# Kernel tuning notes

Hardware: AMD Instinct MI355X
Metric: run time of the kernel (lower is better)

## Reference

```python
import jax, jax.numpy as jnp
import numpy as np

B, S, D, H = 4, 2048, 1024, 16
Dh = D // H
MAX_WAVELENGTH = 10000.0


def apply_rope(x, positions, head_dim):
    # x: [B, S, H, Dh], positions: [B, S]
    fraction = 2.0 * jnp.arange(head_dim // 2, dtype=jnp.float32) / head_dim
    timescale = MAX_WAVELENGTH ** fraction                     # [Dh/2]
    sinusoid = positions[..., None].astype(jnp.float32) / timescale  # [B, S, Dh/2]
    sinusoid = sinusoid[..., None, :]                          # [B, S, 1, Dh/2]
    sin, cos = jnp.sin(sinusoid), jnp.cos(sinusoid)
    first, second = jnp.split(x, 2, axis=-1)
    out = jnp.concatenate([first * cos - second * sin,
                           second * cos + first * sin], axis=-1)
    return out.astype(x.dtype)


def setup_inputs() -> dict:
    key = jax.random.key(0)
    k0, k1, k2, k3, k4 = jax.random.split(key, 5)
    inputs = jax.random.normal(k0, (B, S, D), dtype=jnp.float32)
    segment_positions = jnp.broadcast_to(jnp.arange(S, dtype=jnp.int32), (B, S))
    # causal mask, broadcastable over heads: [B, 1, S, S]
    mask = jnp.broadcast_to(jnp.tril(jnp.ones((S, S), dtype=bool))[None, None], (B, 1, S, S))
    std = 0.02
    w_q = jax.random.normal(k1, (D, H, Dh), dtype=jnp.float32) * std
    w_k = jax.random.normal(k2, (D, H, Dh), dtype=jnp.float32) * std
    w_v = jax.random.normal(k3, (D, H, Dh), dtype=jnp.float32) * std
    w_out = jax.random.normal(k4, (H, Dh, D), dtype=jnp.float32) * std
    return {"inputs": inputs, "w_q": w_q, "w_k": w_k, "w_v": w_v,
            "w_out": w_out, "segment_positions": segment_positions, "mask": mask}


def reference(inputs, w_q, w_k, w_v, w_out, segment_positions, mask):
    # QKV projections: [B, S, D] x [D, H, Dh] -> [B, S, H, Dh]
    q = jnp.einsum('bsd,dhk->bshk', inputs, w_q)
    k = jnp.einsum('bsd,dhk->bshk', inputs, w_k)
    v = jnp.einsum('bsd,dhk->bshk', inputs, w_v)
    q = apply_rope(q, segment_positions, Dh)
    k = apply_rope(k, segment_positions, Dh)
    q = q / jnp.sqrt(jnp.asarray(Dh, dtype=q.dtype))
    attn = jnp.einsum('bqhd,bkhd->bhqk', q, k)                 # [B, H, S, S]
    big_neg = jnp.finfo(attn.dtype).min
    attn = jnp.where(mask, attn, big_neg)
    attn = jax.nn.softmax(attn, axis=-1)
    x = jnp.einsum('bhqk,bkhd->bqhd', attn, v)                 # [B, S, H, Dh]
    return jnp.einsum('bqhd,hdm->bqm', x, w_out)               # [B, S, D]
```

## Files before the change

kernel.cpp:

```cpp
#include <hip/hip_runtime.h>
#include <stdint.h>
#include <math.h>

#define S_LEN 2048
#define DMODEL 1024
#define NHEAD 16
#define DHEAD 64
#define BATCH 4
#define MROWS (BATCH * S_LEN)

typedef __attribute__((ext_vector_type(8))) short bf16x8;
typedef __attribute__((ext_vector_type(4))) float f32x4;

#define MFMA16(a, b, c) __builtin_amdgcn_mfma_f32_16x16x32_bf16(a, b, c, 0, 0, 0)

__device__ __forceinline__ unsigned short f2b(float f) {
  union { float f; unsigned u; } v; v.f = f;
  unsigned u = v.u;
  return (unsigned short)((u + 0x7FFFu + ((u >> 16) & 1u)) >> 16);
}
__device__ __forceinline__ unsigned pkrn(float a, float b) {
  unsigned ua = __float_as_uint(a) + 0x8000u;
  unsigned ub = __float_as_uint(b) + 0x8000u;
  return __builtin_amdgcn_perm(ub, ua, 0x07060302);
}

__device__ __forceinline__ void async16(const void* g, void* l) {
  __builtin_amdgcn_global_load_lds((const __attribute__((address_space(1))) void*)g,
                                   (__attribute__((address_space(3))) void*)l,
                                   16, 0, 0);
}

struct PrepArgs {
  const float4* x; unsigned short* xb; int n4; int cvtBlocks;
  const float* s[4]; unsigned short* d[4];
};
__global__ __launch_bounds__(256) void prep_kernel(PrepArgs p) {
  __shared__ float T[64][65];
  const int bid = blockIdx.x;
  const int t = threadIdx.x;
  if (bid < p.cvtBlocks) {
    int i = bid * 256 + t;
    if (i < p.n4) {
      float4 v = p.x[i];
      ushort4 o;
      o.x = f2b(v.x); o.y = f2b(v.y); o.z = f2b(v.z); o.w = f2b(v.w);
      *(ushort4*)(p.xb + 4 * (size_t)i) = o;
    }
    return;
  }
  const int tb = bid - p.cvtBlocks;
  const int z = tb >> 8;
  const int rem = tb & 255;
  const int r0 = (rem >> 4) * 64, c0 = (rem & 15) * 64;
  const float* in = p.s[z];
  unsigned short* out = p.d[z];
  int c = t & 63, rr = t >> 6;
#pragma unroll
  for (int i = 0; i < 16; i++) {
    int r = i * 4 + rr;
    T[r][c] = in[(size_t)(r0 + r) * 1024 + c0 + c];
  }
  __syncthreads();
  int r2 = t & 63, cc = t >> 6;
#pragma unroll
  for (int i = 0; i < 16; i++) {
    int c2 = i * 4 + cc;
    out[(size_t)(c0 + c2) * 1024 + r0 + r2] = f2b(T[r2][c2]);
  }
}

__global__ __launch_bounds__(256) void gemm_qkv(const unsigned short* __restrict__ A,
                                                const unsigned short* __restrict__ Bt,
                                                unsigned short* __restrict__ Qr,
                                                unsigned short* __restrict__ Kr,
                                                unsigned short* __restrict__ Vt,
                                                const int* __restrict__ pos) {
  constexpr int K = 1024;
  __shared__ unsigned short As[128 * 64];
  __shared__ unsigned short Bs[128 * 64];
  const int bm = blockIdx.y * 128, bn = blockIdx.x * 128;
  const int t = threadIdx.x;
  const int wave = t >> 6, lane = t & 63, quad = lane >> 4, l16 = lane & 15;
  const int wm = (wave >> 1) * 64, wn = (wave & 1) * 64;
  f32x4 acc[4][4] = {};
  const int srow = lane >> 3;
  const int gcol = (((lane & 7) ^ srow)) * 8;
  const unsigned short* Ag = A + (size_t)(bm + wave * 32 + srow) * K + gcol;
  const unsigned short* Bg = Bt + (size_t)(bn + wave * 32 + srow) * K + gcol;
  unsigned short* AsW = &As[(wave * 32) * 64];
  unsigned short* BsW = &Bs[(wave * 32) * 64];
  const int rsw = l16 & 7;

  for (int k0 = 0; k0 < K; k0 += 64) {
    __syncthreads();
#pragma unroll
    for (int i = 0; i < 4; i++) {
      async16(Ag + (size_t)(i * 8) * K + k0, AsW + i * 8 * 64);
      async16(Bg + (size_t)(i * 8) * K + k0, BsW + i * 8 * 64);
    }
    __syncthreads();
#pragma unroll
    for (int kk = 0; kk < 2; kk++) {
      const int sl = ((kk * 4 + quad) ^ rsw) << 3;
      bf16x8 af[4], bfr[4];
#pragma unroll
      for (int mt = 0; mt < 4; mt++)
        af[mt] = *(const bf16x8*)&As[(wm + mt * 16 + l16) * 64 + sl];
#pragma unroll
      for (int nt = 0; nt < 4; nt++)
        bfr[nt] = *(const bf16x8*)&Bs[(wn + nt * 16 + l16) * 64 + sl];
#pragma unroll
      for (int mt = 0; mt < 4; mt++)
#pragma unroll
        for (int nt = 0; nt < 4; nt++)
          acc[mt][nt] = MFMA16(af[mt], bfr[nt], acc[mt][nt]);
    }
  }

  const int cb = bn + wn;
  if (cb >= 2048) {
    const int h = (cb - 2048) >> 6;
#pragma unroll
    for (int mt = 0; mt < 4; mt++)
#pragma unroll
      for (int nt = 0; nt < 4; nt++) {
        int row = bm + wm + mt * 16 + quad * 4;
        int b = row >> 11, s = row & (S_LEN - 1);
        int dh = nt * 16 + l16;
        ushort4 w4;
        w4.x = f2b(acc[mt][nt][0]); w4.y = f2b(acc[mt][nt][1]);
        w4.z = f2b(acc[mt][nt][2]); w4.w = f2b(acc[mt][nt][3]);
        *(ushort4*)&Vt[((size_t)(b * NHEAD + h) * DHEAD + dh) * S_LEN + s] = w4;
      }
  } else {
    const bool isQ = cb < 1024;
    unsigned short* dst0 = isQ ? Qr : Kr;
    const float scl = isQ ? 0.18033688011112042f : 1.0f;
    const int h = (cb >> 6) & 15;
    const float LT = 0.28782313662425572f;
    float it0 = __expf(-(float)l16 * LT);
    float it1 = __expf(-(float)(16 + l16) * LT);
#pragma unroll
    for (int mt = 0; mt < 4; mt++) {
#pragma unroll
      for (int r = 0; r < 4; r++) {
        int row = bm + wm + mt * 16 + quad * 4 + r;
        int b = row >> 11, s = row & (S_LEN - 1);
        float p = (float)pos[row];
        float a0 = p * it0, a1 = p * it1;
        float sn0 = __sinf(a0), cs0 = __cosf(a0);
        float sn1 = __sinf(a1), cs1 = __cosf(a1);
        float x0 = acc[mt][0][r], x1 = acc[mt][1][r];
        float x2 = acc[mt][2][r], x3 = acc[mt][3][r];
        float o0 = (x0 * cs0 - x2 * sn0) * scl;
        float o2 = (x2 * cs0 + x0 * sn0) * scl;
        float o1 = (x1 * cs1 - x3 * sn1) * scl;
        float o3 = (x3 * cs1 + x1 * sn1) * scl;
        unsigned short* dst =
            dst0 + ((size_t)(b * NHEAD + h) * S_LEN + s) * DHEAD;
        dst[0 * 16 + l16] = f2b(o0);
        dst[1 * 16 + l16] = f2b(o1);
        dst[2 * 16 + l16] = f2b(o2);
        dst[3 * 16 + l16] = f2b(o3);
      }
    }
  }
}

__global__ __launch_bounds__(256) void gemm_out(const unsigned short* __restrict__ A,
                                                const unsigned short* __restrict__ Bt,
                                                float* __restrict__ C) {
  constexpr int K = 1024, N = 1024;
  __shared__ unsigned short As[128 * 64];
  __shared__ unsigned short Bs[128 * 64];
  const int bm = blockIdx.y * 128, bn = blockIdx.x * 128;
  const int t = threadIdx.x;
  const int wave = t >> 6, lane = t & 63, quad = lane >> 4, l16 = lane & 15;
  const int wm = (wave >> 1) * 64, wn = (wave & 1) * 64;
  f32x4 acc[4][4] = {};
  const int srow = lane >> 3;
  const int gcol = (((lane & 7) ^ srow)) * 8;
  const unsigned short* Ag = A + (size_t)(bm + wave * 32 + srow) * K + gcol;
  const unsigned short* Bg = Bt + (size_t)(bn + wave * 32 + srow) * K + gcol;
  unsigned short* AsW = &As[(wave * 32) * 64];
  unsigned short* BsW = &Bs[(wave * 32) * 64];
  const int rsw = l16 & 7;

  for (int k0 = 0; k0 < K; k0 += 64) {
    __syncthreads();
#pragma unroll
    for (int i = 0; i < 4; i++) {
      async16(Ag + (size_t)(i * 8) * K + k0, AsW + i * 8 * 64);
      async16(Bg + (size_t)(i * 8) * K + k0, BsW + i * 8 * 64);
    }
    __syncthreads();
#pragma unroll
    for (int kk = 0; kk < 2; kk++) {
      const int sl = ((kk * 4 + quad) ^ rsw) << 3;
      bf16x8 af[4], bfr[4];
#pragma unroll
      for (int mt = 0; mt < 4; mt++)
        af[mt] = *(const bf16x8*)&As[(wm + mt * 16 + l16) * 64 + sl];
#pragma unroll
      for (int nt = 0; nt < 4; nt++)
        bfr[nt] = *(const bf16x8*)&Bs[(wn + nt * 16 + l16) * 64 + sl];
#pragma unroll
      for (int mt = 0; mt < 4; mt++)
#pragma unroll
        for (int nt = 0; nt < 4; nt++)
          acc[mt][nt] = MFMA16(af[mt], bfr[nt], acc[mt][nt]);
    }
  }
#pragma unroll
  for (int mt = 0; mt < 4; mt++)
#pragma unroll
    for (int nt = 0; nt < 4; nt++)
#pragma unroll
      for (int r = 0; r < 4; r++) {
        int row = bm + wm + mt * 16 + quad * 4 + r;
        int col = bn + wn + nt * 16 + l16;
        C[(size_t)row * N + col] = acc[mt][nt][r];
      }
}

__global__ __launch_bounds__(256, 3) void flash_kernel(const unsigned short* __restrict__ Qr,
                                                       const unsigned short* __restrict__ Kr,
                                                       const unsigned short* __restrict__ Vt,
                                                       unsigned short* __restrict__ Xat) {
  const int idx = blockIdx.x;
  const int j = idx >> 6;
  const int bh = idx & 63;
  const int jB = 31 - j;
  const unsigned short* Qh = Qr + (size_t)bh * S_LEN * DHEAD;
  const unsigned short* Kh = Kr + (size_t)bh * S_LEN * DHEAD;
  const unsigned short* Vh = Vt + (size_t)bh * DHEAD * S_LEN;
  __shared__ unsigned short Ks[2][64 * 64];
  __shared__ unsigned short Vs[2][64 * 64];
  __shared__ unsigned short Pt[4][16 * 64];
  const int t = threadIdx.x, wave = t >> 6, lane = t & 63;
  const int quad = lane >> 4, l16 = lane & 15;
  const int srow = lane >> 3;
  const int gcol = (((lane & 7) ^ srow)) * 8;
  const int rsw = l16 & 7;
  const int qrA = j * 64 + wave * 16 + l16;
  const int qrB = jB * 64 + wave * 16 + l16;

  bf16x8 qfA0 = *(const bf16x8*)(Qh + (size_t)qrA * DHEAD + quad * 8);
  bf16x8 qfA1 = *(const bf16x8*)(Qh + (size_t)qrA * DHEAD + 32 + quad * 8);
  bf16x8 qfB0 = *(const bf16x8*)(Qh + (size_t)qrB * DHEAD + quad * 8);
  bf16x8 qfB1 = *(const bf16x8*)(Qh + (size_t)qrB * DHEAD + 32 + quad * 8);

  f32x4 oA[4] = {}, oB[4] = {};
  float lA = 0.f, lB = 0.f;
  unsigned short* PtW = &Pt[wave][0];
  const int c0 = (quad ^ rsw) << 3;
  const int c1 = ((4 + quad) ^ rsw) << 3;
  const int q1b = quad >> 1, qlo4 = (quad & 1) * 4;
  const int pr = l16 * 64;

  auto stage = [&](int kt, int buf) {
    const int k0 = kt * 64;
#pragma unroll
    for (int i = 0; i < 2; i++) {
      async16(Kh + (size_t)(k0 + wave * 16 + i * 8 + srow) * DHEAD + gcol,
              &Ks[buf][(wave * 16 + i * 8) * 64]);
      async16(Vh + (size_t)(wave * 16 + i * 8 + srow) * S_LEN + k0 + gcol,
              &Vs[buf][(wave * 16 + i * 8) * 64]);
    }
  };

  auto softpv = [&](const unsigned short* V_, f32x4* sc, f32x4* o, float& l,
                    int qr_, bool diag, int k0) {
#pragma unroll
    for (int nt = 0; nt < 4; nt++) {
      float p0, p1, p2, p3;
      if (diag) {
        int kg = k0 + nt * 16 + quad * 4;
        p0 = (kg + 0 > qr_) ? 0.f : exp2f(sc[nt][0]);
        p1 = (kg + 1 > qr_) ? 0.f : exp2f(sc[nt][1]);
        p2 = (kg + 2 > qr_) ? 0.f : exp2f(sc[nt][2]);
        p3 = (kg + 3 > qr_) ? 0.f : exp2f(sc[nt][3]);
      } else {
        p0 = exp2f(sc[nt][0]);
        p1 = exp2f(sc[nt][1]);
        p2 = exp2f(sc[nt][2]);
        p3 = exp2f(sc[nt][3]);
      }
      l += (p0 + p1) + (p2 + p3);
      uint2 w; w.x = pkrn(p0, p1); w.y = pkrn(p2, p3);
      const int slot = ((nt * 2 + q1b) ^ rsw) << 3;
      *(uint2*)&PtW[pr + slot + qlo4] = w;
    }
#pragma unroll
    for (int kk = 0; kk < 2; kk++) {
      bf16x8 pb = *(const bf16x8*)&PtW[pr + (((kk * 4 + quad) ^ rsw) << 3)];
#pragma unroll
      for (int nt = 0; nt < 4; nt++) {
        bf16x8 vb = *(const bf16x8*)&V_[(nt * 16 + l16) * 64 + (kk == 0 ? c0 : c1)];
        o[nt] = MFMA16(vb, pb, o[nt]);
      }
    }
  };

  auto computeAB = [&](int cur, int k0, bool adiag) {
    const unsigned short* K_ = Ks[cur];
    const unsigned short* V_ = Vs[cur];
    f32x4 scA[4] = {}, scB[4] = {};
#pragma unroll
    for (int nt = 0; nt < 4; nt++) {
      bf16x8 kb0 = *(const bf16x8*)&K_[(nt * 16 + l16) * 64 + c0];
      bf16x8 kb1 = *(const bf16x8*)&K_[(nt * 16 + l16) * 64 + c1];
      scA[nt] = MFMA16(kb0, qfA0, scA[nt]);
      scA[nt] = MFMA16(kb1, qfA1, scA[nt]);
      scB[nt] = MFMA16(kb0, qfB0, scB[nt]);
      scB[nt] = MFMA16(kb1, qfB1, scB[nt]);
    }
    softpv(V_, scA, oA, lA, qrA, adiag, k0);
    softpv(V_, scB, oB, lB, qrB, false, k0);
  };

  auto computeB = [&](int cur, int k0, bool bdiag) {
    const unsigned short* K_ = Ks[cur];
    const unsigned short* V_ = Vs[cur];
    f32x4 scB[4] = {};
#pragma unroll
    for (int nt = 0; nt < 4; nt++) {
      bf16x8 kb0 = *(const bf16x8*)&K_[(nt * 16 + l16) * 64 + c0];
      bf16x8 kb1 = *(const bf16x8*)&K_[(nt * 16 + l16) * 64 + c1];
      scB[nt] = MFMA16(kb0, qfB0, scB[nt]);
      scB[nt] = MFMA16(kb1, qfB1, scB[nt]);
    }
    softpv(V_, scB, oB, lB, qrB, bdiag, k0);
  };

  stage(0, 0);
  int cur = 0;
  for (int kt = 0; kt < j; ++kt) {
    __syncthreads();
    stage(kt + 1, cur ^ 1);
    computeAB(cur, kt * 64, false);
    cur ^= 1;
  }
  __syncthreads();
  stage(j + 1, cur ^ 1);
  computeAB(cur, j * 64, true);
  cur ^= 1;
  for (int kt = j + 1; kt < jB; ++kt) {
    __syncthreads();
    stage(kt + 1, cur ^ 1);
    computeB(cur, kt * 64, false);
    cur ^= 1;
  }
  __syncthreads();
  computeB(cur, jB * 64, true);

  lA += __shfl_xor(lA, 16); lA += __shfl_xor(lA, 32);
  lB += __shfl_xor(lB, 16); lB += __shfl_xor(lB, 32);
  const float ivA = 1.0f / lA, ivB = 1.0f / lB;
  const int b = bh >> 4, h = bh & 15;
  unsigned short* dA = Xat + (size_t)(b * S_LEN + qrA) * DMODEL + h * DHEAD;
  unsigned short* dB = Xat + (size_t)(b * S_LEN + qrB) * DMODEL + h * DHEAD;
#pragma unroll
  for (int nt = 0; nt < 4; nt++) {
    ushort4 wa, wb;
    wa.x = f2b(oA[nt][0] * ivA); wa.y = f2b(oA[nt][1] * ivA);
    wa.z = f2b(oA[nt][2] * ivA); wa.w = f2b(oA[nt][3] * ivA);
    wb.x = f2b(oB[nt][0] * ivB); wb.y = f2b(oB[nt][1] * ivB);
    wb.z = f2b(oB[nt][2] * ivB); wb.w = f2b(oB[nt][3] * ivB);
    *(ushort4*)(dA + nt * 16 + quad * 4) = wa;
    *(ushort4*)(dB + nt * 16 + quad * 4) = wb;
  }
}

extern "C" void kernel_launch(void* const* d_in, const int* in_sizes, int n_in,
                              void* d_out, int out_size, void* d_ws, size_t ws_size,
                              hipStream_t stream) {
  const float* x = (const float*)d_in[0];
  const float* wq = (const float*)d_in[1];
  const float* wk = (const float*)d_in[2];
  const float* wv = (const float*)d_in[3];
  const float* wo = (const float*)d_in[4];
  const int* pos = (const int*)d_in[5];
  float* out = (float*)d_out;
  char* ws = (char*)d_ws;

  const size_t EL_X = (size_t)MROWS * DMODEL;
  const size_t EL_W = (size_t)DMODEL * DMODEL;
  unsigned short* Xb = (unsigned short*)ws;
  unsigned short* Wqkv = Xb + EL_X;
  unsigned short* WoT = Wqkv + 3 * EL_W;
  unsigned short* Qr = WoT + EL_W;
  unsigned short* Kr = Qr + EL_X;
  unsigned short* Vt = Kr + EL_X;
  unsigned short* Xat = Vt + EL_X;

  PrepArgs pa;
  pa.x = (const float4*)x; pa.xb = Xb;
  pa.n4 = (int)(EL_X / 4);
  pa.cvtBlocks = (int)(EL_X / 4 / 256);
  pa.s[0] = wq; pa.d[0] = Wqkv;
  pa.s[1] = wk; pa.d[1] = Wqkv + EL_W;
  pa.s[2] = wv; pa.d[2] = Wqkv + 2 * EL_W;
  pa.s[3] = wo; pa.d[3] = WoT;
  prep_kernel<<<pa.cvtBlocks + 1024, 256, 0, stream>>>(pa);

  dim3 gq(24, 64);
  gemm_qkv<<<gq, 256, 0, stream>>>(Xb, Wqkv, Qr, Kr, Vt, pos);
  flash_kernel<<<1024, 256, 0, stream>>>(Qr, Kr, Vt, Xat);
  dim3 gg(8, 64);
  gemm_out<<<gg, 256, 0, stream>>>(Xat, WoT, out);
}
```

Measured before the change: 299.0 us.

## Rewrite QKV GEMM as 256x256 pipelined tile and restructure flash query pairing

The QKV projection GEMM moves to 512-thread blocks computing 256x256 tiles with double-buffered async LDS loads staged in quarters, interleaved with MFMA groups under explicit barriers, waitcnts and priority hints. A swizzled block index improves L2 reuse, and the larger tile raises arithmetic intensity per byte loaded. Separately, the flash kernel now pairs two adjacent 64-row query tiles, replacing the first/last tile pairing used for causal load balance, and visits them longest-first. That may reduce K/V reloading but leaves blocks with unequal work. The hand-written waitcnt and barrier scheduling is fragile, and the 64KB of LDS per block may limit occupancy.

```diff
diff --git a/kernel.cpp b/kernel.cpp
--- a/kernel.cpp
+++ b/kernel.cpp
@@ -30,6 +30,15 @@
                                    (__attribute__((address_space(3))) void*)l,
                                    16, 0, 0);
 }
+
+#define BAR() __builtin_amdgcn_s_barrier()
+#define LGKM0()                                        \
+  do {                                                 \
+    asm volatile("s_waitcnt lgkmcnt(0)" ::: "memory"); \
+    __builtin_amdgcn_sched_barrier(0);                 \
+  } while (0)
+#define VMC2() asm volatile("s_waitcnt vmcnt(2)" ::: "memory")
+#define VMC0() asm volatile("s_waitcnt vmcnt(0)" ::: "memory")
 
 struct PrepArgs {
   const float4* x; unsigned short* xb; int n4; int cvtBlocks;
@@ -70,62 +79,126 @@
   }
 }
 
-__global__ __launch_bounds__(256) void gemm_qkv(const unsigned short* __restrict__ A,
-                                                const unsigned short* __restrict__ Bt,
-                                                unsigned short* __restrict__ Qr,
-                                                unsigned short* __restrict__ Kr,
-                                                unsigned short* __restrict__ Vt,
-                                                const int* __restrict__ pos) {
-  constexpr int K = 1024;
-  __shared__ unsigned short As[128 * 64];
-  __shared__ unsigned short Bs[128 * 64];
-  const int bm = blockIdx.y * 128, bn = blockIdx.x * 128;
+#define MFMA_QUAD(MB, NB)                                                     \
+  do {                                                                        \
+    _Pragma("unroll") for (int mi = 0; mi < 4; mi++)                          \
+      _Pragma("unroll") for (int ni = 0; ni < 2; ni++) {                      \
+        acc[(MB) + mi][(NB) + ni] =                                           \
+            MFMA16(af[mi][0], bfr[(NB) + ni][0], acc[(MB) + mi][(NB) + ni]);  \
+        acc[(MB) + mi][(NB) + ni] =                                           \
+            MFMA16(af[mi][1], bfr[(NB) + ni][1], acc[(MB) + mi][(NB) + ni]);  \
+      }                                                                       \
+  } while (0)
+
+__global__ __launch_bounds__(512, 2) void gemm_qkv(const unsigned short* __restrict__ A,
+                                                   const unsigned short* __restrict__ Bt,
+                                                   unsigned short* __restrict__ Qr,
+                                                   unsigned short* __restrict__ Kr,
+                                                   unsigned short* __restrict__ Vt,
+                                                   const int* __restrict__ pos) {
+  constexpr int K = 1024, NT = 16;
+  __shared__ unsigned short As[2][256 * 64];
+  __shared__ unsigned short Bs[2][256 * 64];
+  const int bid = blockIdx.x;
+  const int sw = (bid & 7) * 48 + (bid >> 3);
+  const int bm = (sw / 12) * 256, bn = (sw % 12) * 256;
   const int t = threadIdx.x;
   const int wave = t >> 6, lane = t & 63, quad = lane >> 4, l16 = lane & 15;
-  const int wm = (wave >> 1) * 64, wn = (wave & 1) * 64;
-  f32x4 acc[4][4] = {};
+  const int wr = wave >> 2, wc = wave & 3;
   const int srow = lane >> 3;
-  const int gcol = (((lane & 7) ^ srow)) * 8;
-  const unsigned short* Ag = A + (size_t)(bm + wave * 32 + srow) * K + gcol;
-  const unsigned short* Bg = Bt + (size_t)(bn + wave * 32 + srow) * K + gcol;
-  unsigned short* AsW = &As[(wave * 32) * 64];
-  unsigned short* BsW = &Bs[(wave * 32) * 64];
-  const int rsw = l16 & 7;
-
-  for (int k0 = 0; k0 < K; k0 += 64) {
-    __syncthreads();
-#pragma unroll
-    for (int i = 0; i < 4; i++) {
-      async16(Ag + (size_t)(i * 8) * K + k0, AsW + i * 8 * 64);
-      async16(Bg + (size_t)(i * 8) * K + k0, BsW + i * 8 * 64);
-    }
-    __syncthreads();
-#pragma unroll
-    for (int kk = 0; kk < 2; kk++) {
-      const int sl = ((kk * 4 + quad) ^ rsw) << 3;
-      bf16x8 af[4], bfr[4];
-#pragma unroll
-      for (int mt = 0; mt < 4; mt++)
-        af[mt] = *(const bf16x8*)&As[(wm + mt * 16 + l16) * 64 + sl];
-#pragma unroll
-      for (int nt = 0; nt < 4; nt++)
-        bfr[nt] = *(const bf16x8*)&Bs[(wn + nt * 16 + l16) * 64 + sl];
-#pragma unroll
-      for (int mt = 0; mt < 4; mt++)
-#pragma unroll
-        for (int nt = 0; nt < 4; nt++)
-          acc[mt][nt] = MFMA16(af[mt], bfr[nt], acc[mt][nt]);
-    }
-  }
-
-  const int cb = bn + wn;
+  const int gcol = ((lane & 7) ^ srow) * 8;
+  const int rsw8 = l16 & 7;
+  f32x4 acc[8][4] = {};
+
+  auto stage_half = [&](int tt, int h) {
+    const int b = tt & 1;
+    const int k0 = tt * 64;
+    const int hr = (h & 1) * 128;
+    if (h < 2) {
+      const unsigned short* G = A + (size_t)(bm + hr + wave * 8 + srow) * K + k0 + gcol;
+      unsigned short* L = &As[b][(hr + wave * 8) * 64];
+      async16(G, L);
+      async16(G + (size_t)64 * K, L + 64 * 64);
+    } else {
+      const unsigned short* G = Bt + (size_t)(bn + hr + wave * 8 + srow) * K + k0 + gcol;
+      unsigned short* L = &Bs[b][(hr + wave * 8) * 64];
+      async16(G, L);
+      async16(G + (size_t)64 * K, L + 64 * 64);
+    }
+  };
+  auto ldA = [&](const unsigned short* Ab, int m, int kk) -> bf16x8 {
+    return *(const bf16x8*)&Ab[(wr * 128 + m * 16 + l16) * 64 +
+                               (((kk * 4 + quad) ^ rsw8) << 3)];
+  };
+  auto ldB = [&](const unsigned short* Bb, int n, int kk) -> bf16x8 {
+    return *(const bf16x8*)&Bb[(wc * 64 + n * 16 + l16) * 64 +
+                               (((kk * 4 + quad) ^ rsw8) << 3)];
+  };
+
+  auto ktile = [&](int tt, int smode) {
+    const int b = tt & 1;
+    const unsigned short* Ab = &As[b][0];
+    const unsigned short* Bb = &Bs[b][0];
+    bf16x8 af[4][2], bfr[4][2];
+    if (smode) stage_half(tt + 1, 1);
+#pragma unroll
+    for (int mi = 0; mi < 4; mi++) {
+      af[mi][0] = ldA(Ab, mi, 0); af[mi][1] = ldA(Ab, mi, 1);
+    }
+#pragma unroll
+    for (int ni = 0; ni < 2; ni++) {
+      bfr[ni][0] = ldB(Bb, ni, 0); bfr[ni][1] = ldB(Bb, ni, 1);
+    }
+    BAR(); LGKM0();
+    __builtin_amdgcn_s_setprio(1);
+    MFMA_QUAD(0, 0);
+    __builtin_amdgcn_s_setprio(0);
+    BAR();
+    if (smode) stage_half(tt + 1, 2);
+#pragma unroll
+    for (int ni = 0; ni < 2; ni++) {
+      bfr[2 + ni][0] = ldB(Bb, 2 + ni, 0); bfr[2 + ni][1] = ldB(Bb, 2 + ni, 1);
+    }
+    BAR(); LGKM0();
+    __builtin_amdgcn_s_setprio(1);
+    MFMA_QUAD(0, 2);
+    __builtin_amdgcn_s_setprio(0);
+    BAR();
+    if (smode) stage_half(tt + 1, 3);
+#pragma unroll
+    for (int mi = 0; mi < 4; mi++) {
+      af[mi][0] = ldA(Ab, 4 + mi, 0); af[mi][1] = ldA(Ab, 4 + mi, 1);
+    }
+    BAR(); LGKM0();
+    __builtin_amdgcn_s_setprio(1);
+    MFMA_QUAD(4, 2);
+    __builtin_amdgcn_s_setprio(0);
+    BAR();
+    if (smode == 2) stage_half(tt + 2, 0);
+    BAR();
+    __builtin_amdgcn_s_setprio(1);
+    MFMA_QUAD(4, 0);
+    __builtin_amdgcn_s_setprio(0);
+    if (smode == 2) { VMC2(); } else if (smode == 1) { VMC0(); }
+    BAR();
+  };
+
+  stage_half(0, 0); stage_half(0, 1); stage_half(0, 2); stage_half(0, 3);
+  stage_half(1, 0);
+  VMC2(); BAR();
+
+  for (int tt = 0; tt < NT - 2; ++tt) ktile(tt, 2);
+  ktile(NT - 2, 1);
+  ktile(NT - 1, 0);
+
+  const int cb = bn + wc * 64;
   if (cb >= 2048) {
     const int h = (cb - 2048) >> 6;
 #pragma unroll
-    for (int mt = 0; mt < 4; mt++)
+    for (int mt = 0; mt < 8; mt++)
 #pragma unroll
       for (int nt = 0; nt < 4; nt++) {
-        int row = bm + wm + mt * 16 + quad * 4;
+        int row = bm + wr * 128 + mt * 16 + quad * 4;
         int b = row >> 11, s = row & (S_LEN - 1);
         int dh = nt * 16 + l16;
         ushort4 w4;
@@ -142,10 +215,10 @@
     float it0 = __expf(-(float)l16 * LT);
     float it1 = __expf(-(float)(16 + l16) * LT);
 #pragma unroll
-    for (int mt = 0; mt < 4; mt++) {
+    for (int mt = 0; mt < 8; mt++) {
 #pragma unroll
       for (int r = 0; r < 4; r++) {
-        int row = bm + wm + mt * 16 + quad * 4 + r;
+        int row = bm + wr * 128 + mt * 16 + quad * 4 + r;
         int b = row >> 11, s = row & (S_LEN - 1);
         float p = (float)pos[row];
         float a0 = p * it0, a1 = p * it1;
@@ -229,9 +302,8 @@
                                                        const unsigned short* __restrict__ Vt,
                                                        unsigned short* __restrict__ Xat) {
   const int idx = blockIdx.x;
-  const int j = idx >> 6;
+  const int qt = 15 - (idx >> 6);
   const int bh = idx & 63;
-  const int jB = 31 - j;
   const unsigned short* Qh = Qr + (size_t)bh * S_LEN * DHEAD;
   const unsigned short* Kh = Kr + (size_t)bh * S_LEN * DHEAD;
   const unsigned short* Vh = Vt + (size_t)bh * DHEAD * S_LEN;
@@ -243,8 +315,9 @@
   const int srow = lane >> 3;
   const int gcol = (((lane & 7) ^ srow)) * 8;
   const int rsw = l16 & 7;
-  const int qrA = j * 64 + wave * 16 + l16;
-  const int qrB = jB * 64 + wave * 16 + l16;
+  const int q0 = qt * 128;
+  const int qrA = q0 + wave * 16 + l16;
+  const int qrB = qrA + 64;
 
   bf16x8 qfA0 = *(const bf16x8*)(Qh + (size_t)qrA * DHEAD + quad * 8);
   bf16x8 qfA1 = *(const bf16x8*)(Qh + (size_t)qrA * DHEAD + 32 + quad * 8);
@@ -320,9 +393,24 @@
     softpv(V_, scB, oB, lB, qrB, false, k0);
   };
 
-  auto computeB = [&](int cur, int k0, bool bdiag) {
-    const unsigned short* K_ = Ks[cur];
-    const unsigned short* V_ = Vs[cur];
+  stage(0, 0);
+  const int kmax = 2 * qt;
+  int kt = 0;
+  for (; kt < kmax; kt += 2) {
+    __syncthreads();
+    stage(kt + 1, 1);
+    computeAB(0, kt * 64, false);
+    __syncthreads();
+    stage(kt + 2, 0);
+    computeAB(1, (kt + 1) * 64, false);
+  }
+  __syncthreads();
+  stage(kmax + 1, 1);
+  computeAB(0, kmax * 64, true);
+  __syncthreads();
+  {
+    const unsigned short* K_ = Ks[1];
+    const unsigned short* V_ = Vs[1];
     f32x4 scB[4] = {};
 #pragma unroll
     for (int nt = 0; nt < 4; nt++) {
@@ -331,29 +419,8 @@
       scB[nt] = MFMA16(kb0, qfB0, scB[nt]);
       scB[nt] = MFMA16(kb1, qfB1, scB[nt]);
     }
-    softpv(V_, scB, oB, lB, qrB, bdiag, k0);
-  };
-
-  stage(0, 0);
-  int cur = 0;
-  for (int kt = 0; kt < j; ++kt) {
-    __syncthreads();
-    stage(kt + 1, cur ^ 1);
-    computeAB(cur, kt * 64, false);
-    cur ^= 1;
-  }
-  __syncthreads();
-  stage(j + 1, cur ^ 1);
-  computeAB(cur, j * 64, true);
-  cur ^= 1;
-  for (int kt = j + 1; kt < jB; ++kt) {
-    __syncthreads();
-    stage(kt + 1, cur ^ 1);
-    computeB(cur, kt * 64, false);
-    cur ^= 1;
-  }
-  __syncthreads();
-  computeB(cur, jB * 64, true);
+    softpv(V_, scB, oB, lB, qrB, true, (kmax + 1) * 64);
+  }
 
   lA += __shfl_xor(lA, 16); lA += __shfl_xor(lA, 32);
   lB += __shfl_xor(lB, 16); lB += __shfl_xor(lB, 32);
@@ -405,8 +472,7 @@
   pa.s[3] = wo; pa.d[3] = WoT;
   prep_kernel<<<pa.cvtBlocks + 1024, 256, 0, stream>>>(pa);
 
-  dim3 gq(24, 64);
-  gemm_qkv<<<gq, 256, 0, stream>>>(Xb, Wqkv, Qr, Kr, Vt, pos);
+  gemm_qkv<<<384, 512, 0, stream>>>(Xb, Wqkv, Qr, Kr, Vt, pos);
   flash_kernel<<<1024, 256, 0, stream>>>(Qr, Kr, Vt, Xat);
   dim3 gg(8, 64);
   gemm_out<<<gg, 256, 0, stream>>>(Xat, WoT, out);
```

Measured after the change: 309.3 us. 3.5% more time.
